# Optimization experiments

Hardware: AMD Instinct MI355X
Metric: run time of the kernel (lower is better)

Reference implementation:

```python
import jax, jax.numpy as jnp
import numpy as np

SHIFT = 1  # shift_direction fixed to +1 (original picks +/-1 randomly at init)

def setup_inputs() -> dict:
    key = jax.random.key(0)
    k1, k2, k3 = jax.random.split(key, 3)
    x  = jax.random.normal(k1, (1024, 1792, 28), dtype=jnp.float32)
    w0 = jax.random.normal(k2, (128, 2), dtype=jnp.float32)
    w1 = jax.random.normal(k3, (64, 3, 128), dtype=jnp.float32)
    return {"x": x, "w0": w0, "w1": w1}

def reference(x, w0, w1):
    # unfold (im2col) with kernel (3,1), padding (1,0) along the 28-dim
    xp = jnp.pad(x, ((0, 0), (0, 0), (1, 1)))                 # (1024,1792,30)
    patches = jnp.stack([xp[:, :, k:k + 28] for k in range(3)], axis=2)  # (1024,1792,3,28)
    t3 = patches.reshape(1024, 64, 28, 3, 28)                 # (l,j,m,k,n)
    # einsum 'ljmnk,jki->lmni' (t3 here is in (l,j,m,k,n) order)
    t4 = jnp.einsum('ljmkn,jki->lmni', t3, w1)                # (1024,28,28,128)
    # outer product with w0, directly in the permuted (k,l,i,m,j) order
    t5 = jnp.einsum('klmi,ij->klimj', t4, w0)                 # (1024,28,128,28,2)
    t6 = t5.reshape(1024, 28, 128, 56)
    t6 = jnp.roll(t6, SHIFT, axis=3)
    t6 = t6.reshape(1024, 28, 128, 28, 2).sum(axis=4)         # (1024,28,128,28)
    t7 = jnp.roll(t6, SHIFT, axis=1)
    y = jnp.transpose(t7, (0, 2, 3, 1))                       # (1024,128,28,28)
    return y
```

## Files before the change

### kernel.cpp

```cpp
#include <hip/hip_runtime.h>

typedef short bf16x8 __attribute__((ext_vector_type(8)));
typedef float f32x4 __attribute__((ext_vector_type(4)));
typedef unsigned short u16x4 __attribute__((ext_vector_type(4)));

__device__ __forceinline__ unsigned short f2b(float f) {
    unsigned int u = __builtin_bit_cast(unsigned int, f);
    u += 0x7fffu + ((u >> 16) & 1u);
    return (unsigned short)(u >> 16);
}
__device__ __forceinline__ float b2f(unsigned short s) {
    unsigned int u = ((unsigned int)s) << 16;
    return __builtin_bit_cast(float, u);
}

__global__ void wt_prepass(const float* __restrict__ w1, unsigned short* __restrict__ wt) {
    int t = blockIdx.x * 256 + threadIdx.x;
    if (t >= 24576) return;
    int j = t & 63;
    int i = (t >> 6) & 127;
    int k = t >> 13;
    wt[t] = f2b(w1[(j * 3 + k) * 128 + i]);
}


__global__ __launch_bounds__(512, 4) void fused_main(
        const float* __restrict__ x, const float* __restrict__ w0,
        const unsigned short* __restrict__ wt, float* __restrict__ y) {
    __shared__ __align__(16) char smem[65536];
    __shared__ float w0s[256];

    const int tid  = threadIdx.x;
    const int lane = tid & 63;
    const int w    = tid >> 6;
    const int rl   = lane & 15;
    const int jb0  = (lane >> 4) << 3;

    const int B   = (int)blockIdx.x;
    const int b   = ((B & 7) << 7) + ((B >> 3) >> 2);
    const int bc  = (B >> 3) & 3;
    const int c0  = 7 * bc;

    if (tid < 256) w0s[tid] = w0[tid];

    {
        int nh = (bc == 0) ? 2 : ((bc == 3) ? 1 : 0);
        for (int idx = tid; idx < nh * 224; idx += 512) {
            int rr = idx;
            int sl;
            if (bc == 0) {
                if (rr >= 224) { sl = 11; rr -= 224; } else sl = 0;
            } else {
                sl = 9;
            }
            int a   = rr >> 3, ch = rr & 7;
            int row = a * 13 + sl;
            int byte = (row << 7) + ((ch << 4) ^ ((row & 7) << 4));
            *reinterpret_cast<f32x4*>(smem + byte) = f32x4{0.f, 0.f, 0.f, 0.f};
        }
    }

    int q0, q1, q2;
    if      (bc == 0) { q0 = 0; q1 = 1; q2 = 6; }
    else if (bc == 1) { q0 = 1; q1 = 2; q2 = 3; }
    else if (bc == 2) { q0 = 3; q1 = 4; q2 = 5; }
    else              { q0 = 4; q1 = 5; q2 = 6; }

    const float* xb = x + (size_t)b * (1792 * 28);
    {
        float4 vbuf[11];
#pragma unroll
        for (int u = 0; u < 11; ++u) {
            int f = tid + (u << 9);
            if (f < 5376) {
                int R  = f / 3;
                int q3 = f - R * 3;
                int q  = (q3 == 0) ? q0 : ((q3 == 1) ? q1 : q2);
                vbuf[u] = *reinterpret_cast<const float4*>(xb + R * 28 + (q << 2));
            }
        }
#pragma unroll
        for (int u = 0; u < 11; ++u) {
            int f = tid + (u << 9);
            if (f < 5376) {
                int R  = f / 3;
                int q3 = f - R * 3;
                int q  = (q3 == 0) ? q0 : ((q3 == 1) ? q1 : q2);
                int a  = R % 28;
                int j2 = (R / 28) << 1;
                float vv[4] = {vbuf[u].x, vbuf[u].y, vbuf[u].z, vbuf[u].w};
#pragma unroll
                for (int e = 0; e < 4; ++e) {
                    int n = (q << 2) + e;
                    int sl; bool ok;
                    if (bc == 0) {
                        if (n < 8)        { sl = n + 1;  ok = true; }
                        else if (n >= 26) { sl = n - 17; ok = true; }
                        else              { sl = 0;      ok = false; }
                    } else {
                        sl = n + 2 - c0;
                        ok = (unsigned)sl < 10u;
                    }
                    if (ok) {
                        int row  = a * 13 + sl;
                        int byte = (row << 7) + (j2 ^ ((row & 7) << 4));
                        *(unsigned short*)(smem + byte) = f2b(vv[e]);
                    }
                }
            }
        }
    }
    __syncthreads();

    const int cl  = rl & 7;
    const int rh  = rl >> 3;
    const int mt0 = (w >> 2) * 7;
    const int wn  = w & 3;
    int rowoff[3];
#pragma unroll
    for (int k = 0; k < 3; ++k) {
        int sIdx = (bc == 0) ? ((cl == 0) ? (9 + k) : (cl - 1 + k)) : (cl + k);
        rowoff[k] = rh * 13 + sIdx;
    }

    f32x4 acc[7][2];
#pragma unroll
    for (int mt = 0; mt < 7; ++mt) {
        acc[mt][0] = f32x4{0.f, 0.f, 0.f, 0.f};
        acc[mt][1] = f32x4{0.f, 0.f, 0.f, 0.f};
    }

#pragma unroll
    for (int s = 0; s < 6; ++s) {
        const int k  = s >> 1;
        const int jb = ((s & 1) << 5) + jb0;
        const int jx = jb << 1;
        bf16x8 b0 = *reinterpret_cast<const bf16x8*>(wt + (k << 13) + (((wn << 5) + rl) << 6) + jb);
        bf16x8 b1 = *reinterpret_cast<const bf16x8*>(wt + (k << 13) + (((wn << 5) + 16 + rl) << 6) + jb);
#pragma unroll
        for (int mt = 0; mt < 7; ++mt) {
            int row  = 26 * (mt0 + mt) + rowoff[k];
            int byte = (row << 7) + (jx ^ ((row & 7) << 4));
            bf16x8 af = *reinterpret_cast<const bf16x8*>(smem + byte);
            acc[mt][0] = __builtin_amdgcn_mfma_f32_16x16x32_bf16(af, b0, acc[mt][0], 0, 0, 0);
            acc[mt][1] = __builtin_amdgcn_mfma_f32_16x16x32_bf16(af, b1, acc[mt][1], 0, 0, 0);
        }
    }
    __syncthreads();

    {
        const int rq  = (lane >> 4) << 2;
        const int icb = (wn << 5) + rl;
#pragma unroll
        for (int mt = 0; mt < 7; ++mt) {
            int rbase = ((mt0 + mt) << 4) + rq;
            int a     = rbase >> 3;
            int l     = (a == 27) ? 0 : (a + 1);
            int l2    = l << 1;
            int clb   = rbase & 7;
#pragma unroll
            for (int p = 0; p < 2; ++p) {
                int ic   = icb + (p << 4);
                int base = (ic << 9);
                int ic7  = ic * 7;
#pragma unroll
                for (int q = 0; q < 4; ++q) {
                    int cc   = clb + q;
                    int byte = base + (cc << 6) + (l2 ^ (((ic7 + cc) & 7) << 3));
                    *(unsigned short*)(smem + byte) = f2b(acc[mt][p][q]);
                }
            }
        }
    }
    __syncthreads();

#pragma unroll
    for (int u = 0; u < 13; ++u) {
        int f = tid + (u << 9);
        if (f < 6272) {
            int lq    = f % 7;
            int t1    = f / 7;
            int m_loc = t1 % 7;
            int iloc  = t1 / 7;
            float w00 = w0s[2 * iloc], w01 = w0s[2 * iloc + 1];
            int m     = c0 + m_loc;
            int lo    = lq << 3;
            int i7    = iloc * 7;
            int cl1   = m_loc + 1;
            int cl2   = m_loc;
            int by1   = (iloc << 9) + (cl1 << 6) + (lo ^ (((i7 + cl1) & 7) << 3));
            int by2   = (iloc << 9) + (cl2 << 6) + (lo ^ (((i7 + cl2) & 7) << 3));
            u16x4 h1  = *reinterpret_cast<const u16x4*>(smem + by1);
            u16x4 h2  = *reinterpret_cast<const u16x4*>(smem + by2);
            f32x4 o;
            o.x = w00 * b2f(h1.x) + w01 * b2f(h2.x);
            o.y = w00 * b2f(h1.y) + w01 * b2f(h2.y);
            o.z = w00 * b2f(h1.z) + w01 * b2f(h2.z);
            o.w = w00 * b2f(h1.w) + w01 * b2f(h2.w);
            __builtin_nontemporal_store(
                o, reinterpret_cast<f32x4*>(y + ((((size_t)b * 128 + iloc) * 28 + m) * 28) + (lq << 2)));
        }
    }
}

extern "C" void kernel_launch(void* const* d_in, const int* in_sizes, int n_in,
                              void* d_out, int out_size, void* d_ws, size_t ws_size,
                              hipStream_t stream) {
    const float* x  = (const float*)d_in[0];
    const float* w0 = (const float*)d_in[1];
    const float* w1 = (const float*)d_in[2];
    float* y = (float*)d_out;
    unsigned short* wt = (unsigned short*)d_ws;

    hipLaunchKernelGGL(wt_prepass, dim3(96), dim3(256), 0, stream, w1, wt);
    hipLaunchKernelGGL(fused_main, dim3(4096), dim3(512), 0, stream, x, w0, wt, y);
}
```

Measured before the change: 172.3 us.

## Process two batches per block with prefetch of next batch's input

```diff
diff --git a/kernel.cpp b/kernel.cpp
--- a/kernel.cpp
+++ b/kernel.cpp
@@ -24,10 +24,10 @@
 }
 
 
-__global__ __launch_bounds__(512, 4) void fused_main(
+__global__ __launch_bounds__(512, 2) void fused_main(
         const float* __restrict__ x, const float* __restrict__ w0,
         const unsigned short* __restrict__ wt, float* __restrict__ y) {
-    __shared__ __align__(16) char smem[65536];
+    __shared__ __align__(16) char smem[93184];
     __shared__ float w0s[256];
 
     const int tid  = threadIdx.x;
@@ -37,28 +37,14 @@
     const int jb0  = (lane >> 4) << 3;
 
     const int B   = (int)blockIdx.x;
-    const int b   = ((B & 7) << 7) + ((B >> 3) >> 2);
-    const int bc  = (B >> 3) & 3;
+    const int xcd = B & 7;
+    const int g   = B >> 3;
+    const int bc  = g & 3;
+    const int bp  = g >> 2;
+    const int b0  = (xcd << 7) + (bp << 1);
     const int c0  = 7 * bc;
 
     if (tid < 256) w0s[tid] = w0[tid];
-
-    {
-        int nh = (bc == 0) ? 2 : ((bc == 3) ? 1 : 0);
-        for (int idx = tid; idx < nh * 224; idx += 512) {
-            int rr = idx;
-            int sl;
-            if (bc == 0) {
-                if (rr >= 224) { sl = 11; rr -= 224; } else sl = 0;
-            } else {
-                sl = 9;
-            }
-            int a   = rr >> 3, ch = rr & 7;
-            int row = a * 13 + sl;
-            int byte = (row << 7) + ((ch << 4) ^ ((row & 7) << 4));
-            *reinterpret_cast<f32x4*>(smem + byte) = f32x4{0.f, 0.f, 0.f, 0.f};
-        }
-    }
 
     int q0, q1, q2;
     if      (bc == 0) { q0 = 0; q1 = 1; q2 = 6; }
@@ -66,9 +52,20 @@
     else if (bc == 2) { q0 = 3; q1 = 4; q2 = 5; }
     else              { q0 = 4; q1 = 5; q2 = 6; }
 
-    const float* xb = x + (size_t)b * (1792 * 28);
+    const int cl  = rl & 7;
+    const int rh  = rl >> 3;
+    const int mt0 = (w >> 2) * 7;
+    const int wn  = w & 3;
+    int rowoff[3];
+#pragma unroll
+    for (int k = 0; k < 3; ++k) {
+        int sIdx = (bc == 0) ? ((cl == 0) ? (9 + k) : (cl - 1 + k)) : (cl + k);
+        rowoff[k] = rh * 13 + sIdx;
+    }
+
+    float4 buf[11];
     {
-        float4 vbuf[11];
+        const float* xb = x + (size_t)b0 * 50176;
 #pragma unroll
         for (int u = 0; u < 11; ++u) {
             int f = tid + (u << 9);
@@ -76,9 +73,33 @@
                 int R  = f / 3;
                 int q3 = f - R * 3;
                 int q  = (q3 == 0) ? q0 : ((q3 == 1) ? q1 : q2);
-                vbuf[u] = *reinterpret_cast<const float4*>(xb + R * 28 + (q << 2));
-            }
-        }
+                buf[u] = *reinterpret_cast<const float4*>(xb + R * 28 + (q << 2));
+            }
+        }
+    }
+
+#pragma unroll
+    for (int t = 0; t < 2; ++t) {
+        const int xsb = t ? 46592 : 0;
+        const int b   = b0 + t;
+
+        {
+            int nh = (bc == 0) ? 2 : ((bc == 3) ? 1 : 0);
+            for (int idx = tid; idx < nh * 224; idx += 512) {
+                int rr = idx;
+                int sl;
+                if (bc == 0) {
+                    if (rr >= 224) { sl = 11; rr -= 224; } else sl = 0;
+                } else {
+                    sl = 9;
+                }
+                int a   = rr >> 3, ch = rr & 7;
+                int row = a * 13 + sl;
+                int byte = xsb + (row << 7) + ((ch << 4) ^ ((row & 7) << 4));
+                *reinterpret_cast<f32x4*>(smem + byte) = f32x4{0.f, 0.f, 0.f, 0.f};
+            }
+        }
+
 #pragma unroll
         for (int u = 0; u < 11; ++u) {
             int f = tid + (u << 9);
@@ -88,7 +109,7 @@
                 int q  = (q3 == 0) ? q0 : ((q3 == 1) ? q1 : q2);
                 int a  = R % 28;
                 int j2 = (R / 28) << 1;
-                float vv[4] = {vbuf[u].x, vbuf[u].y, vbuf[u].z, vbuf[u].w};
+                float vv[4] = {buf[u].x, buf[u].y, buf[u].z, buf[u].w};
 #pragma unroll
                 for (int e = 0; e < 4; ++e) {
                     int n = (q << 2) + e;
@@ -103,103 +124,111 @@
                     }
                     if (ok) {
                         int row  = a * 13 + sl;
-                        int byte = (row << 7) + (j2 ^ ((row & 7) << 4));
+                        int byte = xsb + (row << 7) + (j2 ^ ((row & 7) << 4));
                         *(unsigned short*)(smem + byte) = f2b(vv[e]);
                     }
                 }
             }
         }
-    }
-    __syncthreads();
-
-    const int cl  = rl & 7;
-    const int rh  = rl >> 3;
-    const int mt0 = (w >> 2) * 7;
-    const int wn  = w & 3;
-    int rowoff[3];
-#pragma unroll
-    for (int k = 0; k < 3; ++k) {
-        int sIdx = (bc == 0) ? ((cl == 0) ? (9 + k) : (cl - 1 + k)) : (cl + k);
-        rowoff[k] = rh * 13 + sIdx;
-    }
-
-    f32x4 acc[7][2];
-#pragma unroll
-    for (int mt = 0; mt < 7; ++mt) {
-        acc[mt][0] = f32x4{0.f, 0.f, 0.f, 0.f};
-        acc[mt][1] = f32x4{0.f, 0.f, 0.f, 0.f};
-    }
-
-#pragma unroll
-    for (int s = 0; s < 6; ++s) {
-        const int k  = s >> 1;
-        const int jb = ((s & 1) << 5) + jb0;
-        const int jx = jb << 1;
-        bf16x8 b0 = *reinterpret_cast<const bf16x8*>(wt + (k << 13) + (((wn << 5) + rl) << 6) + jb);
-        bf16x8 b1 = *reinterpret_cast<const bf16x8*>(wt + (k << 13) + (((wn << 5) + 16 + rl) << 6) + jb);
+
+        if (t == 0) {
+            const float* xb = x + (size_t)(b0 + 1) * 50176;
+#pragma unroll
+            for (int u = 0; u < 11; ++u) {
+                int f = tid + (u << 9);
+                if (f < 5376) {
+                    int R  = f / 3;
+                    int q3 = f - R * 3;
+                    int q  = (q3 == 0) ? q0 : ((q3 == 1) ? q1 : q2);
+                    buf[u] = *reinterpret_cast<const float4*>(xb + R * 28 + (q << 2));
+                }
+            }
+        }
+
+        asm volatile("s_waitcnt lgkmcnt(0)" ::: "memory");
+        __builtin_amdgcn_s_barrier();
+
+        f32x4 acc[7][2];
 #pragma unroll
         for (int mt = 0; mt < 7; ++mt) {
-            int row  = 26 * (mt0 + mt) + rowoff[k];
-            int byte = (row << 7) + (jx ^ ((row & 7) << 4));
-            bf16x8 af = *reinterpret_cast<const bf16x8*>(smem + byte);
-            acc[mt][0] = __builtin_amdgcn_mfma_f32_16x16x32_bf16(af, b0, acc[mt][0], 0, 0, 0);
-            acc[mt][1] = __builtin_amdgcn_mfma_f32_16x16x32_bf16(af, b1, acc[mt][1], 0, 0, 0);
-        }
-    }
-    __syncthreads();
-
-    {
-        const int rq  = (lane >> 4) << 2;
-        const int icb = (wn << 5) + rl;
-#pragma unroll
-        for (int mt = 0; mt < 7; ++mt) {
-            int rbase = ((mt0 + mt) << 4) + rq;
-            int a     = rbase >> 3;
-            int l     = (a == 27) ? 0 : (a + 1);
-            int l2    = l << 1;
-            int clb   = rbase & 7;
-#pragma unroll
-            for (int p = 0; p < 2; ++p) {
-                int ic   = icb + (p << 4);
-                int base = (ic << 9);
-                int ic7  = ic * 7;
-#pragma unroll
-                for (int q = 0; q < 4; ++q) {
-                    int cc   = clb + q;
-                    int byte = base + (cc << 6) + (l2 ^ (((ic7 + cc) & 7) << 3));
-                    *(unsigned short*)(smem + byte) = f2b(acc[mt][p][q]);
-                }
-            }
-        }
-    }
-    __syncthreads();
-
-#pragma unroll
-    for (int u = 0; u < 13; ++u) {
-        int f = tid + (u << 9);
-        if (f < 6272) {
-            int lq    = f % 7;
-            int t1    = f / 7;
-            int m_loc = t1 % 7;
-            int iloc  = t1 / 7;
-            float w00 = w0s[2 * iloc], w01 = w0s[2 * iloc + 1];
-            int m     = c0 + m_loc;
-            int lo    = lq << 3;
-            int i7    = iloc * 7;
-            int cl1   = m_loc + 1;
-            int cl2   = m_loc;
-            int by1   = (iloc << 9) + (cl1 << 6) + (lo ^ (((i7 + cl1) & 7) << 3));
-            int by2   = (iloc << 9) + (cl2 << 6) + (lo ^ (((i7 + cl2) & 7) << 3));
-            u16x4 h1  = *reinterpret_cast<const u16x4*>(smem + by1);
-            u16x4 h2  = *reinterpret_cast<const u16x4*>(smem + by2);
-            f32x4 o;
-            o.x = w00 * b2f(h1.x) + w01 * b2f(h2.x);
-            o.y = w00 * b2f(h1.y) + w01 * b2f(h2.y);
-            o.z = w00 * b2f(h1.z) + w01 * b2f(h2.z);
-            o.w = w00 * b2f(h1.w) + w01 * b2f(h2.w);
-            __builtin_nontemporal_store(
-                o, reinterpret_cast<f32x4*>(y + ((((size_t)b * 128 + iloc) * 28 + m) * 28) + (lq << 2)));
-        }
+            acc[mt][0] = f32x4{0.f, 0.f, 0.f, 0.f};
+            acc[mt][1] = f32x4{0.f, 0.f, 0.f, 0.f};
+        }
+#pragma unroll
+        for (int s = 0; s < 6; ++s) {
+            const int k  = s >> 1;
+            const int jb = ((s & 1) << 5) + jb0;
+            const int jx = jb << 1;
+            bf16x8 bA = *reinterpret_cast<const bf16x8*>(wt + (k << 13) + (((wn << 5) + rl) << 6) + jb);
+            bf16x8 bB = *reinterpret_cast<const bf16x8*>(wt + (k << 13) + (((wn << 5) + 16 + rl) << 6) + jb);
+#pragma unroll
+            for (int mt = 0; mt < 7; ++mt) {
+                int row  = 26 * (mt0 + mt) + rowoff[k];
+                int byte = xsb + (row << 7) + (jx ^ ((row & 7) << 4));
+                bf16x8 af = *reinterpret_cast<const bf16x8*>(smem + byte);
+                acc[mt][0] = __builtin_amdgcn_mfma_f32_16x16x32_bf16(af, bA, acc[mt][0], 0, 0, 0);
+                acc[mt][1] = __builtin_amdgcn_mfma_f32_16x16x32_bf16(af, bB, acc[mt][1], 0, 0, 0);
+            }
+        }
+        asm volatile("s_waitcnt lgkmcnt(0)" ::: "memory");
+        __builtin_amdgcn_s_barrier();
+
+        {
+            const int rq  = (lane >> 4) << 2;
+            const int icb = (wn << 5) + rl;
+#pragma unroll
+            for (int mt = 0; mt < 7; ++mt) {
+                int rbase = ((mt0 + mt) << 4) + rq;
+                int a     = rbase >> 3;
+                int l     = (a == 27) ? 0 : (a + 1);
+                int l2    = l << 1;
+                int clb   = rbase & 7;
+#pragma unroll
+                for (int p = 0; p < 2; ++p) {
+                    int ic   = icb + (p << 4);
+                    int base = (ic << 9);
+                    int ic7  = ic * 7;
+#pragma unroll
+                    for (int q = 0; q < 4; ++q) {
+                        int cc   = clb + q;
+                        int byte = base + (cc << 6) + (l2 ^ (((ic7 + cc) & 7) << 3));
+                        *(unsigned short*)(smem + byte) = f2b(acc[mt][p][q]);
+                    }
+                }
+            }
+        }
+        asm volatile("s_waitcnt lgkmcnt(0)" ::: "memory");
+        __builtin_amdgcn_s_barrier();
+
+#pragma unroll
+        for (int u = 0; u < 13; ++u) {
+            int f = tid + (u << 9);
+            if (f < 6272) {
+                int lq    = f % 7;
+                int t1    = f / 7;
+                int m_loc = t1 % 7;
+                int iloc  = t1 / 7;
+                float w00 = w0s[2 * iloc], w01 = w0s[2 * iloc + 1];
+                int m     = c0 + m_loc;
+                int lo    = lq << 3;
+                int i7    = iloc * 7;
+                int cl1   = m_loc + 1;
+                int cl2   = m_loc;
+                int by1   = (iloc << 9) + (cl1 << 6) + (lo ^ (((i7 + cl1) & 7) << 3));
+                int by2   = (iloc << 9) + (cl2 << 6) + (lo ^ (((i7 + cl2) & 7) << 3));
+                u16x4 h1  = *reinterpret_cast<const u16x4*>(smem + by1);
+                u16x4 h2  = *reinterpret_cast<const u16x4*>(smem + by2);
+                f32x4 o;
+                o.x = w00 * b2f(h1.x) + w01 * b2f(h2.x);
+                o.y = w00 * b2f(h1.y) + w01 * b2f(h2.y);
+                o.z = w00 * b2f(h1.z) + w01 * b2f(h2.z);
+                o.w = w00 * b2f(h1.w) + w01 * b2f(h2.w);
+                __builtin_nontemporal_store(
+                    o, reinterpret_cast<f32x4*>(y + ((((size_t)b * 128 + iloc) * 28 + m) * 28) + (lq << 2)));
+            }
+        }
+        asm volatile("s_waitcnt lgkmcnt(0)" ::: "memory");
+        __builtin_amdgcn_s_barrier();
     }
 }
 
@@ -213,5 +242,5 @@
     unsigned short* wt = (unsigned short*)d_ws;
 
     hipLaunchKernelGGL(wt_prepass, dim3(96), dim3(256), 0, stream, w1, wt);
-    hipLaunchKernelGGL(fused_main, dim3(4096), dim3(512), 0, stream, x, w0, wt, y);
-}
+    hipLaunchKernelGGL(fused_main, dim3(2048), dim3(512), 0, stream, x, w0, wt, y);
+}
```

Measured after the change: 325.5 us. 88.9% more time.

## Fold w0 into GEMM weights and store accumulators directly to global

Applied to the files above, without the earlier changes.

```diff
diff --git a/kernel.cpp b/kernel.cpp
--- a/kernel.cpp
+++ b/kernel.cpp
@@ -2,33 +2,30 @@
 
 typedef short bf16x8 __attribute__((ext_vector_type(8)));
 typedef float f32x4 __attribute__((ext_vector_type(4)));
-typedef unsigned short u16x4 __attribute__((ext_vector_type(4)));
 
 __device__ __forceinline__ unsigned short f2b(float f) {
     unsigned int u = __builtin_bit_cast(unsigned int, f);
     u += 0x7fffu + ((u >> 16) & 1u);
     return (unsigned short)(u >> 16);
 }
-__device__ __forceinline__ float b2f(unsigned short s) {
-    unsigned int u = ((unsigned int)s) << 16;
-    return __builtin_bit_cast(float, u);
-}
 
-__global__ void wt_prepass(const float* __restrict__ w1, unsigned short* __restrict__ wt) {
+__global__ void w2_prepass(const float* __restrict__ w0, const float* __restrict__ w1,
+                           unsigned short* __restrict__ wab) {
     int t = blockIdx.x * 256 + threadIdx.x;
-    if (t >= 24576) return;
-    int j = t & 63;
-    int i = (t >> 6) & 127;
-    int k = t >> 13;
-    wt[t] = f2b(w1[(j * 3 + k) * 128 + i]);
+    if (t >= 49152) return;
+    int which = (t >= 24576) ? 1 : 0;
+    int u = t - which * 24576;
+    int j = u & 63;
+    int i = (u >> 6) & 127;
+    int k = u >> 13;
+    wab[t] = f2b(w0[2 * i + which] * w1[(j * 3 + k) * 128 + i]);
 }
 
 
 __global__ __launch_bounds__(512, 4) void fused_main(
-        const float* __restrict__ x, const float* __restrict__ w0,
-        const unsigned short* __restrict__ wt, float* __restrict__ y) {
-    __shared__ __align__(16) char smem[65536];
-    __shared__ float w0s[256];
+        const float* __restrict__ x, const unsigned short* __restrict__ wA,
+        const unsigned short* __restrict__ wB, float* __restrict__ y) {
+    __shared__ __align__(16) char smem[46592];
 
     const int tid  = threadIdx.x;
     const int lane = tid & 63;
@@ -40,8 +37,6 @@
     const int b   = ((B & 7) << 7) + ((B >> 3) >> 2);
     const int bc  = (B >> 3) & 3;
     const int c0  = 7 * bc;
-
-    if (tid < 256) w0s[tid] = w0[tid];
 
     {
         int nh = (bc == 0) ? 2 : ((bc == 3) ? 1 : 0);
@@ -112,15 +107,18 @@
     }
     __syncthreads();
 
-    const int cl  = rl & 7;
-    const int rh  = rl >> 3;
-    const int mt0 = (w >> 2) * 7;
-    const int wn  = w & 3;
-    int rowoff[3];
+    const int wn    = w & 3;
+    const int mhalf = w >> 2;
+    int ap13[7], sA[7], sB[7];
 #pragma unroll
-    for (int k = 0; k < 3; ++k) {
-        int sIdx = (bc == 0) ? ((cl == 0) ? (9 + k) : (cl - 1 + k)) : (cl + k);
-        rowoff[k] = rh * 13 + sIdx;
+    for (int mt = 0; mt < 7; ++mt) {
+        int r  = ((mhalf * 7 + mt) << 4) + rl;
+        int ml = r / 28;
+        int l  = r - ml * 28;
+        int ap = (l == 0) ? 27 : l - 1;
+        ap13[mt] = ap * 13;
+        sA[mt] = (bc == 0) ? ml : ml + 1;
+        sB[mt] = (bc == 0) ? ((ml == 0) ? 9 : ml - 1) : ml;
     }
 
     f32x4 acc[7][2];
@@ -131,74 +129,36 @@
     }
 
 #pragma unroll
-    for (int s = 0; s < 6; ++s) {
-        const int k  = s >> 1;
-        const int jb = ((s & 1) << 5) + jb0;
+    for (int st = 0; st < 12; ++st) {
+        const int k  = (st % 6) >> 1;
+        const int jh = st & 1;
+        const int jb = (jh << 5) + jb0;
         const int jx = jb << 1;
-        bf16x8 b0 = *reinterpret_cast<const bf16x8*>(wt + (k << 13) + (((wn << 5) + rl) << 6) + jb);
-        bf16x8 b1 = *reinterpret_cast<const bf16x8*>(wt + (k << 13) + (((wn << 5) + 16 + rl) << 6) + jb);
+        const unsigned short* wp = (st < 6) ? wA : wB;
+        bf16x8 b0 = *reinterpret_cast<const bf16x8*>(wp + (k << 13) + (((wn << 5) + rl) << 6) + jb);
+        bf16x8 b1 = *reinterpret_cast<const bf16x8*>(wp + (k << 13) + (((wn << 5) + 16 + rl) << 6) + jb);
 #pragma unroll
         for (int mt = 0; mt < 7; ++mt) {
-            int row  = 26 * (mt0 + mt) + rowoff[k];
+            int row  = ap13[mt] + ((st < 6) ? sA[mt] : sB[mt]) + k;
             int byte = (row << 7) + (jx ^ ((row & 7) << 4));
             bf16x8 af = *reinterpret_cast<const bf16x8*>(smem + byte);
             acc[mt][0] = __builtin_amdgcn_mfma_f32_16x16x32_bf16(af, b0, acc[mt][0], 0, 0, 0);
             acc[mt][1] = __builtin_amdgcn_mfma_f32_16x16x32_bf16(af, b1, acc[mt][1], 0, 0, 0);
         }
     }
-    __syncthreads();
 
-    {
-        const int rq  = (lane >> 4) << 2;
-        const int icb = (wn << 5) + rl;
+    const int rq  = (lane >> 4) << 2;
+    const int icb = (wn << 5) + rl;
+    float* yb = y + (size_t)b * 100352 + c0 * 28;
 #pragma unroll
-        for (int mt = 0; mt < 7; ++mt) {
-            int rbase = ((mt0 + mt) << 4) + rq;
-            int a     = rbase >> 3;
-            int l     = (a == 27) ? 0 : (a + 1);
-            int l2    = l << 1;
-            int clb   = rbase & 7;
+    for (int mt = 0; mt < 7; ++mt) {
+        int rb = ((mhalf * 7 + mt) << 4) + rq;
+        if (rb < 196) {
 #pragma unroll
             for (int p = 0; p < 2; ++p) {
-                int ic   = icb + (p << 4);
-                int base = (ic << 9);
-                int ic7  = ic * 7;
-#pragma unroll
-                for (int q = 0; q < 4; ++q) {
-                    int cc   = clb + q;
-                    int byte = base + (cc << 6) + (l2 ^ (((ic7 + cc) & 7) << 3));
-                    *(unsigned short*)(smem + byte) = f2b(acc[mt][p][q]);
-                }
+                int ic = icb + (p << 4);
+                *reinterpret_cast<f32x4*>(yb + ic * 784 + rb) = acc[mt][p];
             }
-        }
-    }
-    __syncthreads();
-
-#pragma unroll
-    for (int u = 0; u < 13; ++u) {
-        int f = tid + (u << 9);
-        if (f < 6272) {
-            int lq    = f % 7;
-            int t1    = f / 7;
-            int m_loc = t1 % 7;
-            int iloc  = t1 / 7;
-            float w00 = w0s[2 * iloc], w01 = w0s[2 * iloc + 1];
-            int m     = c0 + m_loc;
-            int lo    = lq << 3;
-            int i7    = iloc * 7;
-            int cl1   = m_loc + 1;
-            int cl2   = m_loc;
-            int by1   = (iloc << 9) + (cl1 << 6) + (lo ^ (((i7 + cl1) & 7) << 3));
-            int by2   = (iloc << 9) + (cl2 << 6) + (lo ^ (((i7 + cl2) & 7) << 3));
-            u16x4 h1  = *reinterpret_cast<const u16x4*>(smem + by1);
-            u16x4 h2  = *reinterpret_cast<const u16x4*>(smem + by2);
-            f32x4 o;
-            o.x = w00 * b2f(h1.x) + w01 * b2f(h2.x);
-            o.y = w00 * b2f(h1.y) + w01 * b2f(h2.y);
-            o.z = w00 * b2f(h1.z) + w01 * b2f(h2.z);
-            o.w = w00 * b2f(h1.w) + w01 * b2f(h2.w);
-            __builtin_nontemporal_store(
-                o, reinterpret_cast<f32x4*>(y + ((((size_t)b * 128 + iloc) * 28 + m) * 28) + (lq << 2)));
         }
     }
 }
@@ -210,8 +170,9 @@
     const float* w0 = (const float*)d_in[1];
     const float* w1 = (const float*)d_in[2];
     float* y = (float*)d_out;
-    unsigned short* wt = (unsigned short*)d_ws;
+    unsigned short* wA = (unsigned short*)d_ws;
+    unsigned short* wB = wA + 24576;
 
-    hipLaunchKernelGGL(wt_prepass, dim3(96), dim3(256), 0, stream, w1, wt);
-    hipLaunchKernelGGL(fused_main, dim3(4096), dim3(512), 0, stream, x, w0, wt, y);
+    hipLaunchKernelGGL(w2_prepass, dim3(192), dim3(256), 0, stream, w0, w1, wA);
+    hipLaunchKernelGGL(fused_main, dim3(4096), dim3(512), 0, stream, x, wA, wB, y);
 }
```

Result: slower. 278.3 us (+61.5%).
